# Kernel tuning notes

Hardware: AMD Instinct MI355X
Metric: run time of the kernel (lower is better)

## Reference

```python
import jax, jax.numpy as jnp
import numpy as np

BS, NUM_PATCH, N_VARS, PATCH_LEN, D_MODEL = 32, 64, 321, 12, 128
TIME_RATIO, FREQ_RATIO = 0.5, 0.4


def setup_inputs() -> dict:
    key = jax.random.key(0)
    ks = jax.random.split(key, 7)
    x = jax.random.normal(ks[0], (BS, NUM_PATCH, N_VARS, PATCH_LEN), jnp.float32)
    W_in = jax.random.normal(ks[1], (PATCH_LEN, D_MODEL), jnp.float32) / np.sqrt(PATCH_LEN)
    b_in = jnp.zeros((D_MODEL,), jnp.float32)
    W_out = jax.random.normal(ks[2], (D_MODEL, PATCH_LEN), jnp.float32) / np.sqrt(D_MODEL)
    b_out = jnp.zeros((PATCH_LEN,), jnp.float32)
    # nn.Parameter(torch.zeros(1,1,1)) in the original; use small random scalars so grads are non-trivial
    time_mask_token = jax.random.normal(ks[3], (), jnp.float32) * 0.02
    freq_mask_token = jax.random.normal(ks[4], (), jnp.float32) * 0.02
    return {"x": x, "W_in": W_in, "b_in": b_in, "W_out": W_out, "b_out": b_out,
            "time_mask_token": time_mask_token, "freq_mask_token": freq_mask_token}


def _scatter_mask(idx, num_patch):
    # idx: [bs, n_vars, k] patch indices to mask (set False). Returns bool [bs, num_patch, n_vars].
    bs, nv, k = idx.shape
    m = jnp.ones((bs, num_patch, nv), dtype=bool)
    b = jnp.arange(bs)[:, None, None]
    v = jnp.arange(nv)[None, :, None]
    return m.at[b, idx, v].set(False)


def reference(x, W_in, b_in, W_out, b_out, time_mask_token, freq_mask_token):
    bs, num_patch, n_vars, patch_len = x.shape

    # patch2emb applied per token (equivalent to the gather-encode path since the
    # projection is pointwise per patch): [bs, np, nv, d_model]
    emb = jnp.einsum('bpvl,ld->bpvd', x, W_in) + b_in

    # ---- time masking: mask patches with highest coefficient of variation ----
    cv = jnp.std(x, axis=-1, ddof=1) / (jnp.mean(x, axis=-1) + 1e-6)  # [bs, np, nv]
    k_t = int(num_patch * TIME_RATIO)
    _, idx_t = jax.lax.top_k(jnp.transpose(cv, (0, 2, 1)), k_t)       # [bs, nv, k_t]
    mask_t = _scatter_mask(idx_t, num_patch)                           # True = keep
    tokens_t = jnp.where(mask_t[..., None], emb, time_mask_token)
    out_t = jnp.einsum('bpvd,dl->bpvl', tokens_t, W_out) + b_out

    # ---- freq masking: mask patches with lowest mean FFT magnitude ----
    mag = jnp.abs(jnp.fft.rfft(x, axis=-1))                            # [bs, np, nv, pl//2+1]
    score = mag.mean(axis=-1)                                          # [bs, np, nv]
    k_f = int(num_patch * FREQ_RATIO)
    _, idx_f = jax.lax.top_k(-jnp.transpose(score, (0, 2, 1)), k_f)    # smallest scores
    mask_f = _scatter_mask(idx_f, num_patch)
    tokens_f = jnp.where(mask_f[..., None], emb, freq_mask_token)
    out_f = jnp.einsum('bpvd,dl->bpvl', tokens_f, W_out) + b_out

    return out_t * 0.5 + out_f * 0.5
```

## Files before the change

### kernel.cpp

```cpp
#include <hip/hip_runtime.h>
#include <math.h>

constexpr int BS = 32, NV = 321, PL = 12, DM = 128;
constexpr int KT = 32;
constexpr int KF = 25;
constexpr int VB = 8;
constexpr int NCHUNK = 41;
constexpr int SST = 72;

__device__ __forceinline__ unsigned ord(float f) {
  unsigned u = __float_as_uint(f);
  return ((int)u < 0) ? ~u : (u | 0x80000000u);
}

__global__ void prep_kernel(const float* __restrict__ W_in,
                            const float* __restrict__ b_in,
                            const float* __restrict__ W_out,
                            const float* __restrict__ b_out,
                            const float* __restrict__ tt,
                            const float* __restrict__ ft,
                            float* __restrict__ prep) {
  int t = threadIdx.x;
  if (t < 144) {
    int i = t / 12, l = t % 12;
    const float4* Wi = (const float4*)(W_in + i * DM);
    float s = 0.f;
#pragma unroll 8
    for (int d4 = 0; d4 < 32; ++d4) {
      float4 a = Wi[d4];
      const float* wo = W_out + d4 * 48 + l;
      s += a.x * wo[0] + a.y * wo[12] + a.z * wo[24] + a.w * wo[36];
    }
    prep[t] = s;
  } else if (t < 168) {
    int l = (t - 144) % 12;
    float cs = 0.f, cb = 0.f;
#pragma unroll 8
    for (int d = 0; d < DM; ++d) {
      float w = W_out[d * 12 + l];
      cs += w;
      cb += b_in[d] * w;
    }
    if (t < 156) {
      prep[144 + l] = cb;
      prep[156 + l] = tt[0] * cs;
    } else {
      prep[168 + l] = ft[0] * cs;
    }
  } else if (t < 180) {
    prep[180 + (t - 168)] = b_out[t - 168];
  }
}

__global__ __launch_bounds__(256) void fused_kernel(
    const float* __restrict__ x, const float* __restrict__ prep,
    float* __restrict__ out) {
  __shared__ float scv[VB * SST];
  __shared__ float sfs[VB * SST];
  __shared__ __align__(16) float spp[192];
  __shared__ unsigned long long smT[VB], smF[VB];

  const int t = threadIdx.x;
  const int chunk = blockIdx.x;
  const int b = blockIdx.y;
  const int v0 = chunk * VB;
  const bool full = (chunk < 40);
  const int nv = full ? VB : 1;

  const float* xb = x + ((size_t)(b * 64) * NV + v0) * PL;

  float xr[2][12];
  int pp[2], vvv[2];
  if (full) {
#pragma unroll
    for (int h = 0; h < 2; ++h) {
      const int j = t + 256 * h;
      const int p = j >> 3, vv = j & 7;
      pp[h] = p;
      vvv[h] = vv;
      const float4* src = (const float4*)(xb + ((size_t)p * NV + vv) * PL);
      float4 a = src[0], bb = src[1], c = src[2];
      xr[h][0] = a.x;  xr[h][1] = a.y;  xr[h][2] = a.z;  xr[h][3] = a.w;
      xr[h][4] = bb.x; xr[h][5] = bb.y; xr[h][6] = bb.z; xr[h][7] = bb.w;
      xr[h][8] = c.x;  xr[h][9] = c.y;  xr[h][10] = c.z; xr[h][11] = c.w;
    }
  } else {
    pp[0] = t & 63;
    vvv[0] = 0;
    pp[1] = 0;
    vvv[1] = 0;
    if (t < 64) {
      const float4* src = (const float4*)(xb + (size_t)t * NV * PL);
      float4 a = src[0], bb = src[1], c = src[2];
      xr[0][0] = a.x;  xr[0][1] = a.y;  xr[0][2] = a.z;  xr[0][3] = a.w;
      xr[0][4] = bb.x; xr[0][5] = bb.y; xr[0][6] = bb.z; xr[0][7] = bb.w;
      xr[0][8] = c.x;  xr[0][9] = c.y;  xr[0][10] = c.z; xr[0][11] = c.w;
    }
  }

  if (t < 192) spp[t] = prep[t];

  const float H = 0.86602540378443864676f;
#pragma unroll
  for (int h = 0; h < 2; ++h) {
    const bool valid = full || (h == 0 && t < 64);
    if (valid) {
      const float* xv = xr[h];
      float s = 0.f;
#pragma unroll
      for (int i = 0; i < 12; ++i) s += xv[i];
      const float m = s * (1.0f / 12.0f);
      float ss = 0.f;
#pragma unroll
      for (int i = 0; i < 12; ++i) {
        float d = xv[i] - m;
        ss += d * d;
      }
      const float cv = sqrtf(ss * (1.0f / 11.0f)) / (m + 1e-6f);

      const float e1 = xv[1] + xv[11], e2 = xv[2] + xv[10], e3 = xv[3] + xv[9],
                  e4 = xv[4] + xv[8], e5 = xv[5] + xv[7];
      const float o1 = xv[1] - xv[11], o2 = xv[2] - xv[10], o3 = xv[3] - xv[9],
                  o4 = xv[4] - xv[8], o5 = xv[5] - xv[7];
      float mag = fabsf(xv[0] + xv[6] + e1 + e2 + e3 + e4 + e5);
      float re = xv[0] - xv[6] + H * (e1 - e5) + 0.5f * (e2 - e4);
      float im = 0.5f * (o1 + o5) + H * (o2 + o4) + o3;
      mag += sqrtf(re * re + im * im);
      re = xv[0] + xv[6] + 0.5f * (e1 + e5) - 0.5f * (e2 + e4) - e3;
      im = H * (o1 + o2 - o4 - o5);
      mag += sqrtf(re * re + im * im);
      re = xv[0] - xv[6] - e2 + e4;
      im = o1 - o3 + o5;
      mag += sqrtf(re * re + im * im);
      re = xv[0] + xv[6] - 0.5f * (e1 + e2 + e4 + e5) + e3;
      im = H * (o1 - o2 + o4 - o5);
      mag += sqrtf(re * re + im * im);
      re = xv[0] - xv[6] + H * (e5 - e1) + 0.5f * (e2 - e4);
      im = 0.5f * (o1 + o5) - H * (o2 + o4) + o3;
      mag += sqrtf(re * re + im * im);
      re = xv[0] + xv[6] - e1 + e2 - e3 + e4 - e5;
      mag += fabsf(re);
      const float fs = mag * (1.0f / 7.0f);

      scv[vvv[h] * SST + pp[h]] = cv;
      sfs[vvv[h] * SST + pp[h]] = fs;
    }
  }
  __syncthreads();

  const int wv = t >> 6, lane = t & 63;
#pragma unroll
  for (int k = 0; k < 2; ++k) {
    const int vv = wv * 2 + k;
    if (vv < nv) {
      const unsigned ut = ord(scv[vv * SST + lane]);
      const unsigned uf = ~ord(sfs[vv * SST + lane]);
      unsigned tht = 0, thf = 0;
#pragma unroll
      for (int bit = 31; bit >= 0; --bit) {
        const unsigned ct = tht | (1u << bit);
        const unsigned cf = thf | (1u << bit);
        const unsigned long long bt = __ballot(ut >= ct);
        const unsigned long long bf = __ballot(uf >= cf);
        if (__popcll(bt) >= KT) tht = ct;
        if (__popcll(bf) >= KF) thf = cf;
      }
      const unsigned long long pre = (1ull << lane) - 1ull;
      const int gt_t = __popcll(__ballot(ut > tht));
      const int rt = __popcll(__ballot(ut == tht) & pre);
      const bool masked_t = (ut > tht) || ((ut == tht) && (rt < KT - gt_t));
      const int gt_f = __popcll(__ballot(uf > thf));
      const int rf = __popcll(__ballot(uf == thf) & pre);
      const bool masked_f = (uf > thf) || ((uf == thf) && (rf < KF - gt_f));
      const unsigned long long bkt = __ballot(!masked_t);
      const unsigned long long bkf = __ballot(!masked_f);
      if (lane == 0) {
        smT[vv] = bkt;
        smF[vv] = bkf;
      }
    }
  }
  __syncthreads();

  float E0[12], E1[12];
#pragma unroll
  for (int l = 0; l < 12; ++l) {
    E0[l] = spp[144 + l];
    E1[l] = spp[144 + l];
  }
  const float4* M4 = (const float4*)spp;
#pragma unroll
  for (int i = 0; i < 12; ++i) {
    float4 m0 = M4[i * 3], m1 = M4[i * 3 + 1], m2 = M4[i * 3 + 2];
    float a0 = xr[0][i], a1 = xr[1][i];
    E0[0] += a0 * m0.x;  E0[1] += a0 * m0.y;
    E0[2] += a0 * m0.z;  E0[3] += a0 * m0.w;
    E0[4] += a0 * m1.x;  E0[5] += a0 * m1.y;
    E0[6] += a0 * m1.z;  E0[7] += a0 * m1.w;
    E0[8] += a0 * m2.x;  E0[9] += a0 * m2.y;
    E0[10] += a0 * m2.z; E0[11] += a0 * m2.w;
    E1[0] += a1 * m0.x;  E1[1] += a1 * m0.y;
    E1[2] += a1 * m0.z;  E1[3] += a1 * m0.w;
    E1[4] += a1 * m1.x;  E1[5] += a1 * m1.y;
    E1[6] += a1 * m1.z;  E1[7] += a1 * m1.w;
    E1[8] += a1 * m2.x;  E1[9] += a1 * m2.y;
    E1[10] += a1 * m2.z; E1[11] += a1 * m2.w;
  }
#pragma unroll
  for (int h = 0; h < 2; ++h) {
    const bool valid = full || (h == 0 && t < 64);
    if (valid) {
      const int p = pp[h], vv = vvv[h];
      const bool kt = (smT[vv] >> p) & 1ull;
      const bool kf = (smF[vv] >> p) & 1ull;
      const float* E = (h == 0) ? E0 : E1;
      float o[12];
#pragma unroll
      for (int l = 0; l < 12; ++l) {
        float e = E[l];
        float at = kt ? e : spp[156 + l];
        float af = kf ? e : spp[168 + l];
        o[l] = 0.5f * (at + af) + spp[180 + l];
      }
      float* op = out + ((size_t)(b * 64 + p) * NV + v0 + vv) * PL;
      ((float4*)op)[0] = make_float4(o[0], o[1], o[2], o[3]);
      ((float4*)op)[1] = make_float4(o[4], o[5], o[6], o[7]);
      ((float4*)op)[2] = make_float4(o[8], o[9], o[10], o[11]);
    }
  }
}

extern "C" void kernel_launch(void* const* d_in, const int* in_sizes, int n_in,
                              void* d_out, int out_size, void* d_ws,
                              size_t ws_size, hipStream_t stream) {
  const float* x = (const float*)d_in[0];
  const float* W_in = (const float*)d_in[1];
  const float* b_in = (const float*)d_in[2];
  const float* W_out = (const float*)d_in[3];
  const float* b_out = (const float*)d_in[4];
  const float* tt = (const float*)d_in[5];
  const float* ft = (const float*)d_in[6];
  float* out = (float*)d_out;
  float* prep = (float*)d_ws;

  hipLaunchKernelGGL(prep_kernel, dim3(1), dim3(192), 0, stream, W_in, b_in,
                     W_out, b_out, tt, ft, prep);
  hipLaunchKernelGGL(fused_kernel, dim3(NCHUNK, BS), dim3(256), 0, stream, x,
                     prep, out);
}
```

Measured before the change: 117.2 us.

## Replace ballot radix-select top-k with per-thread rank counting over 4-variable blocks

Swaps the per-wavefront 32-step ballot bit-search used for top-k thresholding for a direct rank computation. Each thread counts how many of the 64 patch scores are greater than its own, with an index tiebreak, and decides masking from that count. The block now covers 4 variables with one token per thread, giving twice as many blocks, and removes the shared staging of prep weights and the mask bitmasks along with one barrier. The trade is 64 compares per thread for each of the two scores and direct global reads of prep values, in place of the ballot loop. NaN or tie handling may differ slightly from the radix method.

```diff
diff --git a/kernel.cpp b/kernel.cpp
--- a/kernel.cpp
+++ b/kernel.cpp
@@ -4,14 +4,9 @@
 constexpr int BS = 32, NV = 321, PL = 12, DM = 128;
 constexpr int KT = 32;
 constexpr int KF = 25;
-constexpr int VB = 8;
-constexpr int NCHUNK = 41;
+constexpr int VB = 4;
+constexpr int NCHUNK = 81;
 constexpr int SST = 72;
-
-__device__ __forceinline__ unsigned ord(float f) {
-  unsigned u = __float_as_uint(f);
-  return ((int)u < 0) ? ~u : (u | 0x80000000u);
-}
 
 __global__ void prep_kernel(const float* __restrict__ W_in,
                             const float* __restrict__ b_in,
@@ -57,176 +52,112 @@
     float* __restrict__ out) {
   __shared__ float scv[VB * SST];
   __shared__ float sfs[VB * SST];
-  __shared__ __align__(16) float spp[192];
-  __shared__ unsigned long long smT[VB], smF[VB];
 
   const int t = threadIdx.x;
   const int chunk = blockIdx.x;
   const int b = blockIdx.y;
   const int v0 = chunk * VB;
-  const bool full = (chunk < 40);
-  const int nv = full ? VB : 1;
+  const bool full = (chunk < 80);
+  const int p = t >> 2;
+  const int vv = t & 3;
+  const bool valid = full || (vv == 0);
 
-  const float* xb = x + ((size_t)(b * 64) * NV + v0) * PL;
-
-  float xr[2][12];
-  int pp[2], vvv[2];
-  if (full) {
-#pragma unroll
-    for (int h = 0; h < 2; ++h) {
-      const int j = t + 256 * h;
-      const int p = j >> 3, vv = j & 7;
-      pp[h] = p;
-      vvv[h] = vv;
-      const float4* src = (const float4*)(xb + ((size_t)p * NV + vv) * PL);
-      float4 a = src[0], bb = src[1], c = src[2];
-      xr[h][0] = a.x;  xr[h][1] = a.y;  xr[h][2] = a.z;  xr[h][3] = a.w;
-      xr[h][4] = bb.x; xr[h][5] = bb.y; xr[h][6] = bb.z; xr[h][7] = bb.w;
-      xr[h][8] = c.x;  xr[h][9] = c.y;  xr[h][10] = c.z; xr[h][11] = c.w;
-    }
-  } else {
-    pp[0] = t & 63;
-    vvv[0] = 0;
-    pp[1] = 0;
-    vvv[1] = 0;
-    if (t < 64) {
-      const float4* src = (const float4*)(xb + (size_t)t * NV * PL);
-      float4 a = src[0], bb = src[1], c = src[2];
-      xr[0][0] = a.x;  xr[0][1] = a.y;  xr[0][2] = a.z;  xr[0][3] = a.w;
-      xr[0][4] = bb.x; xr[0][5] = bb.y; xr[0][6] = bb.z; xr[0][7] = bb.w;
-      xr[0][8] = c.x;  xr[0][9] = c.y;  xr[0][10] = c.z; xr[0][11] = c.w;
-    }
+  float xr[12];
+  if (valid) {
+    const float4* src =
+        (const float4*)(x + (((size_t)(b * 64 + p) * NV) + v0 + vv) * PL);
+    float4 a = src[0], bb = src[1], c = src[2];
+    xr[0] = a.x;  xr[1] = a.y;  xr[2] = a.z;  xr[3] = a.w;
+    xr[4] = bb.x; xr[5] = bb.y; xr[6] = bb.z; xr[7] = bb.w;
+    xr[8] = c.x;  xr[9] = c.y;  xr[10] = c.z; xr[11] = c.w;
   }
 
-  if (t < 192) spp[t] = prep[t];
+  float cv = 0.f, fs = 0.f;
+  const float H = 0.86602540378443864676f;
+  if (valid) {
+    const float* xv = xr;
+    float s = 0.f;
+#pragma unroll
+    for (int i = 0; i < 12; ++i) s += xv[i];
+    const float m = s * (1.0f / 12.0f);
+    float ss = 0.f;
+#pragma unroll
+    for (int i = 0; i < 12; ++i) {
+      float d = xv[i] - m;
+      ss += d * d;
+    }
+    cv = sqrtf(ss * (1.0f / 11.0f)) / (m + 1e-6f);
 
-  const float H = 0.86602540378443864676f;
-#pragma unroll
-  for (int h = 0; h < 2; ++h) {
-    const bool valid = full || (h == 0 && t < 64);
-    if (valid) {
-      const float* xv = xr[h];
-      float s = 0.f;
-#pragma unroll
-      for (int i = 0; i < 12; ++i) s += xv[i];
-      const float m = s * (1.0f / 12.0f);
-      float ss = 0.f;
-#pragma unroll
-      for (int i = 0; i < 12; ++i) {
-        float d = xv[i] - m;
-        ss += d * d;
-      }
-      const float cv = sqrtf(ss * (1.0f / 11.0f)) / (m + 1e-6f);
+    const float e1 = xv[1] + xv[11], e2 = xv[2] + xv[10], e3 = xv[3] + xv[9],
+                e4 = xv[4] + xv[8], e5 = xv[5] + xv[7];
+    const float o1 = xv[1] - xv[11], o2 = xv[2] - xv[10], o3 = xv[3] - xv[9],
+                o4 = xv[4] - xv[8], o5 = xv[5] - xv[7];
+    float mag = fabsf(xv[0] + xv[6] + e1 + e2 + e3 + e4 + e5);
+    float re = xv[0] - xv[6] + H * (e1 - e5) + 0.5f * (e2 - e4);
+    float im = 0.5f * (o1 + o5) + H * (o2 + o4) + o3;
+    mag += sqrtf(re * re + im * im);
+    re = xv[0] + xv[6] + 0.5f * (e1 + e5) - 0.5f * (e2 + e4) - e3;
+    im = H * (o1 + o2 - o4 - o5);
+    mag += sqrtf(re * re + im * im);
+    re = xv[0] - xv[6] - e2 + e4;
+    im = o1 - o3 + o5;
+    mag += sqrtf(re * re + im * im);
+    re = xv[0] + xv[6] - 0.5f * (e1 + e2 + e4 + e5) + e3;
+    im = H * (o1 - o2 + o4 - o5);
+    mag += sqrtf(re * re + im * im);
+    re = xv[0] - xv[6] + H * (e5 - e1) + 0.5f * (e2 - e4);
+    im = 0.5f * (o1 + o5) - H * (o2 + o4) + o3;
+    mag += sqrtf(re * re + im * im);
+    re = xv[0] + xv[6] - e1 + e2 - e3 + e4 - e5;
+    mag += fabsf(re);
+    fs = mag * (1.0f / 7.0f);
 
-      const float e1 = xv[1] + xv[11], e2 = xv[2] + xv[10], e3 = xv[3] + xv[9],
-                  e4 = xv[4] + xv[8], e5 = xv[5] + xv[7];
-      const float o1 = xv[1] - xv[11], o2 = xv[2] - xv[10], o3 = xv[3] - xv[9],
-                  o4 = xv[4] - xv[8], o5 = xv[5] - xv[7];
-      float mag = fabsf(xv[0] + xv[6] + e1 + e2 + e3 + e4 + e5);
-      float re = xv[0] - xv[6] + H * (e1 - e5) + 0.5f * (e2 - e4);
-      float im = 0.5f * (o1 + o5) + H * (o2 + o4) + o3;
-      mag += sqrtf(re * re + im * im);
-      re = xv[0] + xv[6] + 0.5f * (e1 + e5) - 0.5f * (e2 + e4) - e3;
-      im = H * (o1 + o2 - o4 - o5);
-      mag += sqrtf(re * re + im * im);
-      re = xv[0] - xv[6] - e2 + e4;
-      im = o1 - o3 + o5;
-      mag += sqrtf(re * re + im * im);
-      re = xv[0] + xv[6] - 0.5f * (e1 + e2 + e4 + e5) + e3;
-      im = H * (o1 - o2 + o4 - o5);
-      mag += sqrtf(re * re + im * im);
-      re = xv[0] - xv[6] + H * (e5 - e1) + 0.5f * (e2 - e4);
-      im = 0.5f * (o1 + o5) - H * (o2 + o4) + o3;
-      mag += sqrtf(re * re + im * im);
-      re = xv[0] + xv[6] - e1 + e2 - e3 + e4 - e5;
-      mag += fabsf(re);
-      const float fs = mag * (1.0f / 7.0f);
-
-      scv[vvv[h] * SST + pp[h]] = cv;
-      sfs[vvv[h] * SST + pp[h]] = fs;
-    }
+    scv[vv * SST + p] = cv;
+    sfs[vv * SST + p] = fs;
   }
   __syncthreads();
 
-  const int wv = t >> 6, lane = t & 63;
+  int gt_t = 0, eqb_t = 0, gt_f = 0, eqb_f = 0;
+  if (valid) {
+    const float4* rc = (const float4*)(scv + vv * SST);
+    const float4* rf = (const float4*)(sfs + vv * SST);
 #pragma unroll
-  for (int k = 0; k < 2; ++k) {
-    const int vv = wv * 2 + k;
-    if (vv < nv) {
-      const unsigned ut = ord(scv[vv * SST + lane]);
-      const unsigned uf = ~ord(sfs[vv * SST + lane]);
-      unsigned tht = 0, thf = 0;
-#pragma unroll
-      for (int bit = 31; bit >= 0; --bit) {
-        const unsigned ct = tht | (1u << bit);
-        const unsigned cf = thf | (1u << bit);
-        const unsigned long long bt = __ballot(ut >= ct);
-        const unsigned long long bf = __ballot(uf >= cf);
-        if (__popcll(bt) >= KT) tht = ct;
-        if (__popcll(bf) >= KF) thf = cf;
-      }
-      const unsigned long long pre = (1ull << lane) - 1ull;
-      const int gt_t = __popcll(__ballot(ut > tht));
-      const int rt = __popcll(__ballot(ut == tht) & pre);
-      const bool masked_t = (ut > tht) || ((ut == tht) && (rt < KT - gt_t));
-      const int gt_f = __popcll(__ballot(uf > thf));
-      const int rf = __popcll(__ballot(uf == thf) & pre);
-      const bool masked_f = (uf > thf) || ((uf == thf) && (rf < KF - gt_f));
-      const unsigned long long bkt = __ballot(!masked_t);
-      const unsigned long long bkf = __ballot(!masked_f);
-      if (lane == 0) {
-        smT[vv] = bkt;
-        smF[vv] = bkf;
-      }
+    for (int q4 = 0; q4 < 16; ++q4) {
+      const float4 c4 = rc[q4];
+      const float4 f4 = rf[q4];
+      const int q = q4 * 4;
+      gt_t += (c4.x > cv) + (c4.y > cv) + (c4.z > cv) + (c4.w > cv);
+      gt_f += (f4.x < fs) + (f4.y < fs) + (f4.z < fs) + (f4.w < fs);
+      eqb_t += ((c4.x == cv) & (q + 0 < p)) + ((c4.y == cv) & (q + 1 < p)) +
+               ((c4.z == cv) & (q + 2 < p)) + ((c4.w == cv) & (q + 3 < p));
+      eqb_f += ((f4.x == fs) & (q + 0 < p)) + ((f4.y == fs) & (q + 1 < p)) +
+               ((f4.z == fs) & (q + 2 < p)) + ((f4.w == fs) & (q + 3 < p));
     }
   }
-  __syncthreads();
+  const bool kt = (gt_t + eqb_t) >= KT;
+  const bool kf = (gt_f + eqb_f) >= KF;
 
-  float E0[12], E1[12];
+  float E[12];
 #pragma unroll
-  for (int l = 0; l < 12; ++l) {
-    E0[l] = spp[144 + l];
-    E1[l] = spp[144 + l];
-  }
-  const float4* M4 = (const float4*)spp;
+  for (int l = 0; l < 12; ++l) E[l] = prep[144 + l];
 #pragma unroll
   for (int i = 0; i < 12; ++i) {
-    float4 m0 = M4[i * 3], m1 = M4[i * 3 + 1], m2 = M4[i * 3 + 2];
-    float a0 = xr[0][i], a1 = xr[1][i];
-    E0[0] += a0 * m0.x;  E0[1] += a0 * m0.y;
-    E0[2] += a0 * m0.z;  E0[3] += a0 * m0.w;
-    E0[4] += a0 * m1.x;  E0[5] += a0 * m1.y;
-    E0[6] += a0 * m1.z;  E0[7] += a0 * m1.w;
-    E0[8] += a0 * m2.x;  E0[9] += a0 * m2.y;
-    E0[10] += a0 * m2.z; E0[11] += a0 * m2.w;
-    E1[0] += a1 * m0.x;  E1[1] += a1 * m0.y;
-    E1[2] += a1 * m0.z;  E1[3] += a1 * m0.w;
-    E1[4] += a1 * m1.x;  E1[5] += a1 * m1.y;
-    E1[6] += a1 * m1.z;  E1[7] += a1 * m1.w;
-    E1[8] += a1 * m2.x;  E1[9] += a1 * m2.y;
-    E1[10] += a1 * m2.z; E1[11] += a1 * m2.w;
+    const float a = xr[i];
+#pragma unroll
+    for (int l = 0; l < 12; ++l) E[l] += a * prep[i * 12 + l];
   }
+  if (valid) {
+    float o[12];
 #pragma unroll
-  for (int h = 0; h < 2; ++h) {
-    const bool valid = full || (h == 0 && t < 64);
-    if (valid) {
-      const int p = pp[h], vv = vvv[h];
-      const bool kt = (smT[vv] >> p) & 1ull;
-      const bool kf = (smF[vv] >> p) & 1ull;
-      const float* E = (h == 0) ? E0 : E1;
-      float o[12];
-#pragma unroll
-      for (int l = 0; l < 12; ++l) {
-        float e = E[l];
-        float at = kt ? e : spp[156 + l];
-        float af = kf ? e : spp[168 + l];
-        o[l] = 0.5f * (at + af) + spp[180 + l];
-      }
-      float* op = out + ((size_t)(b * 64 + p) * NV + v0 + vv) * PL;
-      ((float4*)op)[0] = make_float4(o[0], o[1], o[2], o[3]);
-      ((float4*)op)[1] = make_float4(o[4], o[5], o[6], o[7]);
-      ((float4*)op)[2] = make_float4(o[8], o[9], o[10], o[11]);
+    for (int l = 0; l < 12; ++l) {
+      const float at = kt ? E[l] : prep[156 + l];
+      const float af = kf ? E[l] : prep[168 + l];
+      o[l] = 0.5f * (at + af) + prep[180 + l];
     }
+    float* op = out + (((size_t)(b * 64 + p) * NV) + v0 + vv) * PL;
+    ((float4*)op)[0] = make_float4(o[0], o[1], o[2], o[3]);
+    ((float4*)op)[1] = make_float4(o[4], o[5], o[6], o[7]);
+    ((float4*)op)[2] = make_float4(o[8], o[9], o[10], o[11]);
   }
 }
 
```

Measured after the change: 130.3 us. +11.1%, slower.
